# Performance work log

Measured on AMD Instinct MI355X. Metric: run time of the kernel, lower is better.

The kernel has to match this reference:

```python
import jax, jax.numpy as jnp
import numpy as np

B, S, H = 2, 4096, 2048          # batch, seq_len, hidden_size
NH, D, W = 8, 128, 4             # num_kv_heads, head_dim, conv_kernel_size (window)
KD = NH * D                      # key_dim == value_dim == 1024
ROPE_BASE = 1000000.0
EPS = 1e-6


def _rope_tables(d, end, base):
    inv = 1.0 / (base ** (np.arange(0, d, 2)[: d // 2].astype(np.float32) / d))
    f = np.outer(np.arange(end, dtype=np.float32), inv)  # [end, d/2]
    return jnp.asarray(np.cos(f)), jnp.asarray(np.sin(f))


def _apply_rope(x, cos, sin):
    # x: [B,S,h,d]; llama-style interleaved pairs (2i, 2i+1)
    x0, x1 = x[..., 0::2], x[..., 1::2]
    c = cos[None, :, None, :]
    s = sin[None, :, None, :]
    o0 = x0 * c - x1 * s
    o1 = x0 * s + x1 * c
    return jnp.stack([o0, o1], axis=-1).reshape(x.shape)


def setup_inputs() -> dict:
    key = jax.random.key(0)
    ks = jax.random.split(key, 7)
    sd = lambda k, shape, fan_in: jax.random.normal(k, shape, jnp.float32) * (fan_in ** -0.5)
    return {
        "x": jax.random.normal(ks[0], (B, S, H), jnp.float32),
        "W_qkv": sd(ks[1], (H, 3 * KD), H),
        "W_z": sd(ks[2], (H, KD), H),
        "W_b": sd(ks[3], (H, NH), H),
        "W_a": sd(ks[4], (H, NH), H),
        "norm_w": jnp.ones((KD,), jnp.float32),
        "W_out": sd(ks[5], (KD, H), KD),
    }


def _forward(x, W_qkv, W_z, W_b, W_a, norm_w, W_out):
    cos, sin = _rope_tables(D, S, ROPE_BASE)
    qkv = x @ W_qkv
    q, k, v = qkv[..., :KD], qkv[..., KD:2 * KD], qkv[..., 2 * KD:]
    z = x @ W_z           # [B,S,KD]
    bg = x @ W_b          # [B,S,NH]
    ag = x @ W_a          # [B,S,NH]

    q4 = _apply_rope(q.reshape(B, S, NH, D), cos, sin)
    k4 = _apply_rope(k.reshape(B, S, NH, D), cos, sin)
    v4 = v.reshape(B, S, NH, D)

    # Windowed gated delta rule: out[i] = sum_{j=i-W..i} (q_i.k_j/sqrt(D)) * sigmoid(a_i*b_j) * v_j
    # Implemented per diagonal offset (W+1 small, fixed) -- never materializes an SxS matrix.
    scale = 1.0 / np.sqrt(D).astype(np.float32)
    out = jnp.zeros_like(v4)
    idx = jnp.arange(S)
    for off in range(W + 1):
        if off == 0:
            kj, vj, bj = k4, v4, bg
        else:
            kj = jnp.pad(k4, ((0, 0), (off, 0), (0, 0), (0, 0)))[:, :S]
            vj = jnp.pad(v4, ((0, 0), (off, 0), (0, 0), (0, 0)))[:, :S]
            bj = jnp.pad(bg, ((0, 0), (off, 0), (0, 0)))[:, :S]
        score = jnp.einsum('bshd,bshd->bsh', q4, kj) * scale
        s = score * jax.nn.sigmoid(ag * bj)
        s = jnp.where((idx >= off)[None, :, None], s, 0.0)
        out = out + s[..., None] * vj
    # position 0 bypasses the attention entirely: output[0] = v[0]
    out = out.at[:, 0].set(v4[:, 0])

    y = out.reshape(B, S, KD) * jax.nn.sigmoid(z)
    # GatedRMSNorm(y, z): rmsnorm(y) * weight * silu(z)
    yf = y.reshape(B * S, KD)
    zf = z.reshape(B * S, KD)
    rms = jnp.sqrt(jnp.mean(yf * yf, axis=-1, keepdims=True) + EPS)
    yn = (yf / rms) * norm_w * (zf * jax.nn.sigmoid(zf))
    return yn.reshape(B, S, KD) @ W_out


def reference(x, W_qkv, W_z, W_b, W_a, norm_w, W_out):
    return _forward(x, W_qkv, W_z, W_b, W_a, norm_w, W_out)
```

## Files before the change

### kernel.cpp

```cpp
#include <hip/hip_runtime.h>
#include <hip/hip_bf16.h>
#include <stdint.h>

#define B_   2
#define S_   4096
#define H_   2048
#define NH_  8
#define D_   128
#define KD_  1024
#define MR   (B_ * S_)
#define NQKVZ 4096

typedef __attribute__((ext_vector_type(8))) short bf16x8;
typedef __attribute__((ext_vector_type(4))) float f32x4;

__device__ __forceinline__ short f2bf(float f) {
    union { float f; uint32_t u; } v; v.f = f;
    uint32_t r = v.u + 0x7FFF + ((v.u >> 16) & 1);
    return (short)(r >> 16);
}
__device__ __forceinline__ float bf2f(unsigned short u) {
    union { uint32_t u; float f; } v; v.u = (uint32_t)u << 16; return v.f;
}

__device__ __forceinline__ void async_ld16(const void* g, void* l) {
    __builtin_amdgcn_global_load_lds(
        (const __attribute__((address_space(1))) uint32_t*)g,
        (__attribute__((address_space(3))) uint32_t*)l, 16, 0, 0);
}

__global__ __launch_bounds__(256) void k_wba(const float* __restrict__ Wb,
                                             const float* __restrict__ Wa,
                                             float* __restrict__ Wba) {
    int idx = blockIdx.x * 256 + threadIdx.x;
    int k = idx & 2047, c = idx >> 11;
    float v = (c < 8) ? Wb[(size_t)k * 8 + c] : Wa[(size_t)k * 8 + (c - 8)];
    Wba[(size_t)c * 2048 + k] = v;
}

__global__ __launch_bounds__(256) void k_cvt_bgag4(const float* __restrict__ x,
                                                   short* __restrict__ xb,
                                                   const float* __restrict__ Wba,
                                                   float* __restrict__ bgag) {
    const int m0 = blockIdx.x * 4, t = threadIdx.x;
    __shared__ float xs[4][2048];
    __shared__ float part[4][256];
#pragma unroll
    for (int rr = 0; rr < 4; rr++) {
        const float4* xr = (const float4*)(x + (size_t)(m0 + rr) * H_);
        float4 a = xr[t], b = xr[t + 256];
        ((float4*)xs[rr])[t] = a;
        ((float4*)xs[rr])[t + 256] = b;
        short4 oa, ob;
        oa.x = f2bf(a.x); oa.y = f2bf(a.y); oa.z = f2bf(a.z); oa.w = f2bf(a.w);
        ob.x = f2bf(b.x); ob.y = f2bf(b.y); ob.z = f2bf(b.z); ob.w = f2bf(b.w);
        short4* xo = (short4*)(xb + (size_t)(m0 + rr) * H_);
        xo[t] = oa;
        xo[t + 256] = ob;
    }
    __syncthreads();
    const int c = t & 15, seg = t >> 4;
    const int kb = seg * 128;
    const float4* W4 = (const float4*)(Wba + (size_t)c * 2048 + kb);
    const float4* x0 = (const float4*)&xs[0][kb];
    const float4* x1 = (const float4*)&xs[1][kb];
    const float4* x2 = (const float4*)&xs[2][kb];
    const float4* x3 = (const float4*)&xs[3][kb];
    float a0 = 0.f, a1 = 0.f, a2 = 0.f, a3 = 0.f;
#pragma unroll 8
    for (int k4 = 0; k4 < 32; k4++) {
        float4 w = W4[k4];
        float4 v0 = x0[k4], v1 = x1[k4], v2 = x2[k4], v3 = x3[k4];
        a0 += w.x * v0.x + w.y * v0.y + w.z * v0.z + w.w * v0.w;
        a1 += w.x * v1.x + w.y * v1.y + w.z * v1.z + w.w * v1.w;
        a2 += w.x * v2.x + w.y * v2.y + w.z * v2.z + w.w * v2.w;
        a3 += w.x * v3.x + w.y * v3.y + w.z * v3.z + w.w * v3.w;
    }
    part[0][t] = a0; part[1][t] = a1; part[2][t] = a2; part[3][t] = a3;
    __syncthreads();
    if (t < 64) {
        int rr = t >> 4, cc = t & 15;
        float s = 0.f;
#pragma unroll
        for (int j = 0; j < 16; j++) s += part[rr][j * 16 + cc];
        bgag[(size_t)(m0 + rr) * 16 + cc] = s;
    }
}

__global__ __launch_bounds__(256) void k_transpose_cvt(const float* __restrict__ W,
                                                       short* __restrict__ Wt,
                                                       int K, int N) {
    __shared__ float tile[32][33];
    int n0 = blockIdx.x * 32, k0 = blockIdx.y * 32;
    int tx = threadIdx.x, ty = threadIdx.y;
#pragma unroll
    for (int i = 0; i < 32; i += 8)
        tile[ty + i][tx] = W[(size_t)(k0 + ty + i) * N + n0 + tx];
    __syncthreads();
#pragma unroll
    for (int i = 0; i < 32; i += 8)
        Wt[(size_t)(n0 + ty + i) * K + k0 + tx] = f2bf(tile[tx][ty + i]);
}

__global__ __launch_bounds__(256) void k_ropetab(float2* __restrict__ ctab) {
    int idx = blockIdx.x * 256 + threadIdx.x;
    int i = idx & 63, s = idx >> 6;
    float inv = exp2f(-(float)i * (2.0f / 128.0f) * 19.931568569324174f);
    float f = (float)s * inv;
    float sn, cs;
    sincosf(f, &sn, &cs);
    ctab[idx] = make_float2(cs, sn);
}

#define PHASE_TAIL() \
    __builtin_amdgcn_s_setprio(0); \
    asm volatile("s_waitcnt vmcnt(%0)" :: "n"(2 + LB) : "memory"); \
    asm volatile("s_barrier" ::: "memory")
#define LDB_P(SET, BASE, KH) \
    _Pragma("unroll") for (int j = 0; j < NF; j++) \
        bf##SET[j] = *(const bf16x8*)((BASE) + 2 * AHB + (KH) * BHB + (wn + j * 16 + mrow) * 64 + kcA)
#define LDA03_P(SET, BASE, KH) \
    _Pragma("unroll") for (int i = 0; i < 4; i++) \
        af##SET[i] = *(const bf16x8*)((BASE) + (KH) * AHB + (wm + i * 16 + mrow) * 64 + kcA)
#define LDA47_S(BASE, KH) \
    _Pragma("unroll") for (int i = 0; i < 4; i++) \
        afS[i] = *(const bf16x8*)((BASE) + (KH) * AHB + (wm + 64 + i * 16 + mrow) * 64 + kcA)
#define MFMA_PH(SET) \
    _Pragma("unroll") for (int i = 0; i < 4; i++) \
    _Pragma("unroll") for (int j = 0; j < NF; j++) \
        acc[i][j] = __builtin_amdgcn_mfma_f32_16x16x32_bf16(af##SET[i], bf##SET[j], acc[i][j], 0, 0, 0); \
    _Pragma("unroll") for (int i = 0; i < 4; i++) \
    _Pragma("unroll") for (int j = 0; j < NF; j++) \
        acc[4 + i][j] = __builtin_amdgcn_mfma_f32_16x16x32_bf16(afS[i], bf##SET[j], acc[4 + i][j], 0, 0, 0)

template <int BN, int EPI>
__global__ __launch_bounds__(512, 2) void k_gemm256(const short* __restrict__ A,
                                                    const short* __restrict__ Bt,
                                                    float* __restrict__ Cf,
                                                    unsigned short* __restrict__ Cb,
                                                    const float2* __restrict__ ctab,
                                                    int M, int N, int K) {
    constexpr int BM = 256;
    constexpr int NF = BN / 64;
    constexpr int LB = BN / 128;
    constexpr int AHB = BM * 64;
    constexpr int BHB = BN * 64;
    constexpr int BUFB = 2 * AHB + 2 * BHB;
    constexpr int LDSB = (EPI == 0) ? 133120 : 2 * BUFB;
    __shared__ __align__(16) char lds[LDSB];

    const int t = threadIdx.x;
    const int lane = t & 63, wave = t >> 6;
    const int mrow = lane & 15;
    const int kcA = (((lane >> 4) ^ ((mrow >> 1) & 3)) * 16);

    const int nwg = gridDim.x;
    const int w0 = blockIdx.x;
    const int wg = (w0 & 7) * (nwg >> 3) + (w0 >> 3);
    const int NB = N / BN;
    const int bn = (wg % NB) * BN;
    const int bm = (wg / NB) * BM;

    const int wm = (wave >> 2) * 128;
    const int wn = (wave & 3) * (BN / 4);

    const short* __restrict__ Ab = A + (size_t)bm * K;
    const short* __restrict__ Bb = Bt + (size_t)bn * K;

    int aoff[2], adst[2];
#pragma unroll
    for (int l = 0; l < 2; l++) {
        int c = t + l * 512;
        int row = c >> 2;
        int kcg = (c & 3) ^ ((row >> 1) & 3);
        aoff[l] = row * K + kcg * 8;
        adst[l] = c * 16;
    }
    int boff[LB], bdst[LB];
#pragma unroll
    for (int l = 0; l < LB; l++) {
        int c = t + l * 512;
        int row = c >> 2;
        int kcg = (c & 3) ^ ((row >> 1) & 3);
        boff[l] = row * K + kcg * 8;
        bdst[l] = c * 16;
    }

    const int NT = K >> 6;

    auto stageA = [&](int kt, int kh, int p) {
        const short* g = Ab + kt * 64 + kh * 32;
        char* d = lds + p * BUFB + kh * AHB;
#pragma unroll
        for (int l = 0; l < 2; l++) async_ld16(g + aoff[l], d + adst[l]);
    };
    auto stageB = [&](int kt, int kh, int p) {
        const short* g = Bb + kt * 64 + kh * 32;
        char* d = lds + p * BUFB + 2 * AHB + kh * BHB;
#pragma unroll
        for (int l = 0; l < LB; l++) async_ld16(g + boff[l], d + bdst[l]);
    };

    f32x4 acc[8][NF] = {};
    bf16x8 afE[4], bfE[NF], afO[4], bfO[NF], afS[4];

    stageA(0, 0, 0); stageB(0, 0, 0);
    stageA(0, 1, 0); stageB(0, 1, 0);
    {
        int k1 = (NT > 1) ? 1 : 0;
        stageA(k1, 0, 1); stageB(k1, 0, 1);
    }
    asm volatile("s_waitcnt vmcnt(%0)" :: "n"(2 * (2 + LB)) : "memory");
    asm volatile("s_barrier" ::: "memory");
    LDB_P(E, lds, 0); LDA03_P(E, lds, 0);
    asm volatile("s_waitcnt vmcnt(%0)" :: "n"(2 + LB) : "memory");
    asm volatile("s_barrier" ::: "memory");

    for (int kt = 0; kt < NT; kt++) {
        const int p = kt & 1;
        const char* base = lds + p * BUFB;
        const char* baseN = lds + (p ^ 1) * BUFB;
        const int k1 = (kt + 1 < NT) ? (kt + 1) : (NT - 1);
        const int k2 = (kt + 2 < NT) ? (kt + 2) : (NT - 1);

        LDA47_S(base, 0);
        LDB_P(O, base, 1); LDA03_P(O, base, 1);
        stageA(k1, 1, p ^ 1); stageB(k1, 1, p ^ 1);
        __builtin_amdgcn_sched_barrier(0);
        __builtin_amdgcn_s_setprio(1);
        MFMA_PH(E);
        PHASE_TAIL();

        LDA47_S(base, 1);
        LDB_P(E, baseN, 0); LDA03_P(E, baseN, 0);
        stageA(k2, 0, p); stageB(k2, 0, p);
        __builtin_amdgcn_sched_barrier(0);
        __builtin_amdgcn_s_setprio(1);
        MFMA_PH(O);
        PHASE_TAIL();
    }
    asm volatile("s_waitcnt vmcnt(0)" ::: "memory");

    const int crow = (lane >> 4) * 4, ccol = lane & 15;
    if (EPI == 0) {
        float* lf = (float*)lds;
#pragma unroll
        for (int p2 = 0; p2 < 2; p2++) {
            __syncthreads();
#pragma unroll
            for (int i = 0; i < 4; i++) {
                const int ii = p2 * 4 + i;
#pragma unroll
                for (int j = 0; j < NF; j++)
#pragma unroll
                    for (int r = 0; r < 4; r++) {
                        int rl = wm + ii * 16 + crow + r;
                        int slot = (rl & 63) | ((rl >> 7) << 6);
                        lf[slot * 260 + wn + j * 16 + ccol] = acc[ii][j][r];
                    }
            }
            __syncthreads();
#pragma unroll
            for (int rep = 0; rep < 16; rep++) {
                int idx = rep * 512 + t;
                int slot = idx >> 6, c4 = idx & 63;
                int rl = (slot & 63) + p2 * 64 + ((slot >> 6) << 7);
                float4 v = *(const float4*)&lf[slot * 260 + c4 * 4];
                *(float4*)(Cf + (size_t)(bm + rl) * N + bn + c4 * 4) = v;
            }
        }
    } else {
#pragma unroll
        for (int i = 0; i < 8; i++)
#pragma unroll
            for (int j = 0; j < NF; j++) {
                const int col = bn + wn + j * 16 + ccol;
                const int rowb = bm + wm + i * 16 + crow;
                const bool qk = col < 2048;
                const int fi = (col & 127) >> 1;
                const bool even = (col & 1) == 0;
                uint32_t* Cd = (uint32_t*)(Cb + ((size_t)rowb * N + (col & ~1)));
#pragma unroll
                for (int r = 0; r < 4; r++) {
                    float v = acc[i][j][r];
                    if (qk) {
                        int s = (rowb + r) & (S_ - 1);
                        float2 cs = ctab[s * 64 + fi];
                        float pp = __shfl_xor(v, 1);
                        v = even ? v * cs.x - pp * cs.y : v * cs.x + pp * cs.y;
                    }
                    int hb = (int)(unsigned short)f2bf(v);
                    int pb = __shfl_xor(hb, 1);
                    if (even)
                        Cd[(size_t)r * (N >> 1)] = (uint32_t)(hb | (pb << 16));
                }
            }
    }
}

__global__ __launch_bounds__(256) void k_attn(const unsigned short* __restrict__ qkvz,
                                              const float* __restrict__ bgag,
                                              const float* __restrict__ norm_w,
                                              short* __restrict__ yn) {
    const int m = blockIdx.x;
    const int s = m & (S_ - 1);
    const int t = threadIdx.x;
    __shared__ unsigned short kvls[5][2048];
    __shared__ unsigned short qzls[2048];
    __shared__ float sc[NH_][5];
    __shared__ float red[4];
    const int nOff = (s < 4 ? s : 4) + 1;

    for (int off = 0; off < 5; off++) {
        if (off < nOff) {
            const ushort4* r = (const ushort4*)(qkvz + (size_t)(m - off) * NQKVZ + 1024);
            ushort4* d = (ushort4*)kvls[off];
            d[t] = r[t];
            d[t + 256] = r[t + 256];
        }
    }
    {
        const unsigned short* r = qkvz + (size_t)m * NQKVZ;
        ushort4* d = (ushort4*)qzls;
        d[t] = ((const ushort4*)r)[t];
        d[256 + t] = ((const ushort4*)(r + 3072))[t];
    }
    __syncthreads();

    {
        const int h = t >> 5, l = t & 31;
        float qv[4];
#pragma unroll
        for (int d = 0; d < 4; d++) qv[d] = bf2f(qzls[h * 128 + l * 4 + d]);
        const float ag = bgag[(size_t)m * 16 + 8 + h];
#pragma unroll
        for (int off = 0; off < 5; off++) {
            float acc = 0.f;
            if (off < nOff) {
#pragma unroll
                for (int d = 0; d < 4; d++)
                    acc += qv[d] * bf2f(kvls[off][h * 128 + l * 4 + d]);
            }
#pragma unroll
            for (int w = 1; w < 32; w <<= 1) acc += __shfl_xor(acc, w);
            if (l == 0) {
                float val = 0.f;
                if (off < nOff) {
                    float bg = bgag[(size_t)(m - off) * 16 + h];
                    float g = 1.f / (1.f + expf(-ag * bg));
                    val = acc * 0.08838834764831845f * g;
                }
                sc[h][off] = val;
            }
        }
    }
    __syncthreads();

    const int e0 = t * 4, h = e0 >> 7;
    float o[4] = {0.f, 0.f, 0.f, 0.f};
    if (s == 0) {
#pragma unroll
        for (int d = 0; d < 4; d++) o[d] = bf2f(kvls[0][1024 + e0 + d]);
    } else {
        for (int off = 0; off < nOff; off++) {
            float w = sc[h][off];
#pragma unroll
            for (int d = 0; d < 4; d++) o[d] += w * bf2f(kvls[off][1024 + e0 + d]);
        }
    }
    float y[4], zs4[4], ss = 0.f;
#pragma unroll
    for (int d = 0; d < 4; d++) {
        float z = bf2f(qzls[1024 + e0 + d]);
        float sg = 1.f / (1.f + expf(-z));
        y[d] = o[d] * sg;
        zs4[d] = z * sg;
        ss += y[d] * y[d];
    }
    const int wave = t >> 6, lane = t & 63;
#pragma unroll
    for (int w = 1; w < 64; w <<= 1) ss += __shfl_xor(ss, w);
    if (lane == 0) red[wave] = ss;
    __syncthreads();
    float tot = red[0] + red[1] + red[2] + red[3];
    float rinv = 1.f / sqrtf(tot * (1.0f / 1024.0f) + 1e-6f);
    short4 ov;
    ov.x = f2bf(y[0] * rinv * norm_w[e0 + 0] * zs4[0]);
    ov.y = f2bf(y[1] * rinv * norm_w[e0 + 1] * zs4[1]);
    ov.z = f2bf(y[2] * rinv * norm_w[e0 + 2] * zs4[2]);
    ov.w = f2bf(y[3] * rinv * norm_w[e0 + 3] * zs4[3]);
    ((short4*)yn)[(size_t)m * 256 + t] = ov;
}

extern "C" void kernel_launch(void* const* d_in, const int* in_sizes, int n_in,
                              void* d_out, int out_size, void* d_ws, size_t ws_size,
                              hipStream_t stream) {
    const float* x      = (const float*)d_in[0];
    const float* W_qkv  = (const float*)d_in[1];
    const float* W_z    = (const float*)d_in[2];
    const float* W_b    = (const float*)d_in[3];
    const float* W_a    = (const float*)d_in[4];
    const float* norm_w = (const float*)d_in[5];
    const float* W_out  = (const float*)d_in[6];
    float* out = (float*)d_out;

    char* ws = (char*)d_ws;
    short* xb    = (short*)ws;          ws += (size_t)MR * H_ * 2;
    short* Wt1   = (short*)ws;          ws += (size_t)NQKVZ * H_ * 2;
    short* Wt2   = (short*)ws;          ws += (size_t)H_ * KD_ * 2;
    unsigned short* qkvzb = (unsigned short*)ws; ws += (size_t)MR * NQKVZ * 2;
    float* bgag  = (float*)ws;          ws += (size_t)MR * 16 * 4;
    short* yn    = (short*)ws;          ws += (size_t)MR * KD_ * 2;
    float2* ctab = (float2*)ws;         ws += (size_t)S_ * 64 * 8;
    float* Wba   = (float*)ws;          ws += (size_t)16 * 2048 * 4;

    k_wba<<<16 * 2048 / 256, 256, 0, stream>>>(W_b, W_a, Wba);
    k_cvt_bgag4<<<MR / 4, 256, 0, stream>>>(x, xb, Wba, bgag);
    k_transpose_cvt<<<dim3(3072 / 32, 2048 / 32), dim3(32, 8), 0, stream>>>(W_qkv, Wt1, 2048, 3072);
    k_transpose_cvt<<<dim3(1024 / 32, 2048 / 32), dim3(32, 8), 0, stream>>>(W_z, Wt1 + (size_t)3072 * 2048, 2048, 1024);
    k_transpose_cvt<<<dim3(2048 / 32, 1024 / 32), dim3(32, 8), 0, stream>>>(W_out, Wt2, 1024, 2048);
    k_ropetab<<<S_ * 64 / 256, 256, 0, stream>>>(ctab);
    k_gemm256<256, 1><<<(MR / 256) * (NQKVZ / 256), 512, 0, stream>>>(
        xb, Wt1, nullptr, qkvzb, ctab, MR, NQKVZ, H_);
    k_attn<<<MR, 256, 0, stream>>>(qkvzb, bgag, norm_w, yn);
    k_gemm256<256, 0><<<(MR / 256) * (H_ / 256), 512, 0, stream>>>(
        yn, Wt2, out, nullptr, nullptr, MR, H_, KD_);
}
```

Before: 450.9 us.

## Process four rows per block in windowed attention to reuse K/V rows

The attention/norm kernel now handles four consecutive sequence positions per block. It loads 8 K/V rows (4 of halo plus 4 current) into shared memory once instead of up to 5 rows per position, which cuts redundant global reads of neighbouring K/V rows by roughly 2.5x. Q and z are read straight from global memory instead of being staged, and the per-position norm reduction is batched. In exchange each thread holds more registers and each block does more serial work, and the grid is four times smaller.

```diff
diff --git a/kernel.cpp b/kernel.cpp
--- a/kernel.cpp
+++ b/kernel.cpp
@@ -298,98 +298,114 @@
     }
 }
 
-__global__ __launch_bounds__(256) void k_attn(const unsigned short* __restrict__ qkvz,
-                                              const float* __restrict__ bgag,
-                                              const float* __restrict__ norm_w,
-                                              short* __restrict__ yn) {
-    const int m = blockIdx.x;
-    const int s = m & (S_ - 1);
+__global__ __launch_bounds__(256) void k_attn4(const unsigned short* __restrict__ qkvz,
+                                               const float* __restrict__ bgag,
+                                               const float* __restrict__ norm_w,
+                                               short* __restrict__ yn) {
+    const int m0 = blockIdx.x * 4;
+    const int s0 = m0 & (S_ - 1);
     const int t = threadIdx.x;
-    __shared__ unsigned short kvls[5][2048];
-    __shared__ unsigned short qzls[2048];
-    __shared__ float sc[NH_][5];
-    __shared__ float red[4];
-    const int nOff = (s < 4 ? s : 4) + 1;
-
-    for (int off = 0; off < 5; off++) {
-        if (off < nOff) {
-            const ushort4* r = (const ushort4*)(qkvz + (size_t)(m - off) * NQKVZ + 1024);
-            ushort4* d = (ushort4*)kvls[off];
-            d[t] = r[t];
-            d[t + 256] = r[t + 256];
+    __shared__ unsigned short kvls[8][2048];
+    __shared__ float sc[4][NH_][5];
+    __shared__ float red[4][4];
+
+#pragma unroll
+    for (int i = 0; i < 8; i++) {
+        int g = m0 - 4 + i;
+        g = (g < 0) ? 0 : g;
+        const uint4* src = (const uint4*)(qkvz + (size_t)g * NQKVZ + 1024);
+        ((uint4*)kvls[i])[t] = src[t];
+    }
+    __syncthreads();
+
+    {
+        const int r = t >> 6, h = (t >> 3) & 7, l8 = t & 7;
+        const int sr = s0 + r;
+        const int nOff = (sr < 4 ? sr : 4) + 1;
+        float qv[16];
+        {
+            const unsigned short* qg = qkvz + (size_t)(m0 + r) * NQKVZ + h * 128 + l8 * 16;
+#pragma unroll
+            for (int d = 0; d < 16; d++) qv[d] = bf2f(qg[d]);
         }
-    }
-    {
-        const unsigned short* r = qkvz + (size_t)m * NQKVZ;
-        ushort4* d = (ushort4*)qzls;
-        d[t] = ((const ushort4*)r)[t];
-        d[256 + t] = ((const ushort4*)(r + 3072))[t];
-    }
-    __syncthreads();
-
-    {
-        const int h = t >> 5, l = t & 31;
-        float qv[4];
-#pragma unroll
-        for (int d = 0; d < 4; d++) qv[d] = bf2f(qzls[h * 128 + l * 4 + d]);
-        const float ag = bgag[(size_t)m * 16 + 8 + h];
+        const float ag = bgag[(size_t)(m0 + r) * 16 + 8 + h];
 #pragma unroll
         for (int off = 0; off < 5; off++) {
             float acc = 0.f;
-            if (off < nOff) {
-#pragma unroll
-                for (int d = 0; d < 4; d++)
-                    acc += qv[d] * bf2f(kvls[off][h * 128 + l * 4 + d]);
-            }
-#pragma unroll
-            for (int w = 1; w < 32; w <<= 1) acc += __shfl_xor(acc, w);
-            if (l == 0) {
+            const unsigned short* kk = kvls[r + 4 - off] + h * 128 + l8 * 16;
+#pragma unroll
+            for (int d = 0; d < 16; d++) acc += qv[d] * bf2f(kk[d]);
+#pragma unroll
+            for (int w = 1; w < 8; w <<= 1) acc += __shfl_xor(acc, w);
+            if (l8 == 0) {
                 float val = 0.f;
                 if (off < nOff) {
-                    float bg = bgag[(size_t)(m - off) * 16 + h];
+                    float bg = bgag[(size_t)(m0 + r - off) * 16 + h];
                     float g = 1.f / (1.f + expf(-ag * bg));
                     val = acc * 0.08838834764831845f * g;
                 }
-                sc[h][off] = val;
+                sc[r][h][off] = val;
             }
         }
     }
     __syncthreads();
 
-    const int e0 = t * 4, h = e0 >> 7;
-    float o[4] = {0.f, 0.f, 0.f, 0.f};
-    if (s == 0) {
-#pragma unroll
-        for (int d = 0; d < 4; d++) o[d] = bf2f(kvls[0][1024 + e0 + d]);
-    } else {
-        for (int off = 0; off < nOff; off++) {
-            float w = sc[h][off];
-#pragma unroll
-            for (int d = 0; d < 4; d++) o[d] += w * bf2f(kvls[off][1024 + e0 + d]);
+    const int e0 = t * 4, h2 = t >> 5;
+    float yv[4][4], zs[4][4], ssr[4];
+    float nw[4];
+    {
+        const float4 n4 = *(const float4*)(norm_w + e0);
+        nw[0] = n4.x; nw[1] = n4.y; nw[2] = n4.z; nw[3] = n4.w;
+    }
+#pragma unroll
+    for (int r = 0; r < 4; r++) {
+        const int sr = s0 + r;
+        float o[4] = {0.f, 0.f, 0.f, 0.f};
+        if (sr == 0) {
+#pragma unroll
+            for (int d = 0; d < 4; d++) o[d] = bf2f(kvls[r + 4][1024 + e0 + d]);
+        } else {
+            const int nOff = (sr < 4 ? sr : 4) + 1;
+            for (int off = 0; off < nOff; off++) {
+                float w = sc[r][h2][off];
+#pragma unroll
+                for (int d = 0; d < 4; d++)
+                    o[d] += w * bf2f(kvls[r + 4 - off][1024 + e0 + d]);
+            }
         }
-    }
-    float y[4], zs4[4], ss = 0.f;
-#pragma unroll
-    for (int d = 0; d < 4; d++) {
-        float z = bf2f(qzls[1024 + e0 + d]);
-        float sg = 1.f / (1.f + expf(-z));
-        y[d] = o[d] * sg;
-        zs4[d] = z * sg;
-        ss += y[d] * y[d];
+        const unsigned short* zg = qkvz + (size_t)(m0 + r) * NQKVZ + 3072 + e0;
+        float ss = 0.f;
+#pragma unroll
+        for (int d = 0; d < 4; d++) {
+            float z = bf2f(zg[d]);
+            float sg = 1.f / (1.f + expf(-z));
+            yv[r][d] = o[d] * sg;
+            zs[r][d] = z * sg;
+            ss += yv[r][d] * yv[r][d];
+        }
+        ssr[r] = ss;
     }
     const int wave = t >> 6, lane = t & 63;
 #pragma unroll
-    for (int w = 1; w < 64; w <<= 1) ss += __shfl_xor(ss, w);
-    if (lane == 0) red[wave] = ss;
-    __syncthreads();
-    float tot = red[0] + red[1] + red[2] + red[3];
-    float rinv = 1.f / sqrtf(tot * (1.0f / 1024.0f) + 1e-6f);
-    short4 ov;
-    ov.x = f2bf(y[0] * rinv * norm_w[e0 + 0] * zs4[0]);
-    ov.y = f2bf(y[1] * rinv * norm_w[e0 + 1] * zs4[1]);
-    ov.z = f2bf(y[2] * rinv * norm_w[e0 + 2] * zs4[2]);
-    ov.w = f2bf(y[3] * rinv * norm_w[e0 + 3] * zs4[3]);
-    ((short4*)yn)[(size_t)m * 256 + t] = ov;
+    for (int r = 0; r < 4; r++)
+#pragma unroll
+        for (int w = 1; w < 64; w <<= 1) ssr[r] += __shfl_xor(ssr[r], w);
+    if (lane == 0) {
+        red[wave][0] = ssr[0]; red[wave][1] = ssr[1];
+        red[wave][2] = ssr[2]; red[wave][3] = ssr[3];
+    }
+    __syncthreads();
+#pragma unroll
+    for (int r = 0; r < 4; r++) {
+        float tot = red[0][r] + red[1][r] + red[2][r] + red[3][r];
+        float rinv = 1.f / sqrtf(tot * (1.0f / 1024.0f) + 1e-6f);
+        short4 ov;
+        ov.x = f2bf(yv[r][0] * rinv * nw[0] * zs[r][0]);
+        ov.y = f2bf(yv[r][1] * rinv * nw[1] * zs[r][1]);
+        ov.z = f2bf(yv[r][2] * rinv * nw[2] * zs[r][2]);
+        ov.w = f2bf(yv[r][3] * rinv * nw[3] * zs[r][3]);
+        ((short4*)yn)[(size_t)(m0 + r) * 256 + t] = ov;
+    }
 }
 
 extern "C" void kernel_launch(void* const* d_in, const int* in_sizes, int n_in,
@@ -422,7 +438,7 @@
     k_ropetab<<<S_ * 64 / 256, 256, 0, stream>>>(ctab);
     k_gemm256<256, 1><<<(MR / 256) * (NQKVZ / 256), 512, 0, stream>>>(
         xb, Wt1, nullptr, qkvzb, ctab, MR, NQKVZ, H_);
-    k_attn<<<MR, 256, 0, stream>>>(qkvzb, bgag, norm_w, yn);
+    k_attn4<<<MR / 4, 256, 0, stream>>>(qkvzb, bgag, norm_w, yn);
     k_gemm256<256, 0><<<(MR / 256) * (H_ / 256), 512, 0, stream>>>(
         yn, Wt2, out, nullptr, nullptr, MR, H_, KD_);
 }
```

New measurement: 440.1 us. -2.4%, faster.
